# Kernel tuning notes

Hardware: AMD Instinct MI355X
Metric: run time of the kernel (lower is better)

Reference implementation:

```python
import jax, jax.numpy as jnp
import numpy as np

N = 50000      # nodes (B-rep faces)
E = 800000     # directed edges (avg degree 16)
F_IN = 9       # 8 surface-type flags + is_feature
H1, H2, C = 512, 128, 2


def setup_inputs() -> dict:
    key = jax.random.key(0)
    ks = jax.random.split(key, 8)
    x = jax.random.normal(ks[0], (N, F_IN), dtype=jnp.float32)
    edge_index = jax.random.randint(ks[1], (2, E), 0, N, dtype=jnp.int64)
    W1 = jax.random.normal(ks[2], (F_IN, H1), dtype=jnp.float32) / np.sqrt(F_IN)
    b1 = jnp.zeros((H1,), dtype=jnp.float32)
    W2 = jax.random.normal(ks[3], (H1, H2), dtype=jnp.float32) / np.sqrt(H1)
    b2 = jnp.zeros((H2,), dtype=jnp.float32)
    W3 = jax.random.normal(ks[4], (H2, C), dtype=jnp.float32) / np.sqrt(H2)
    b3 = jnp.zeros((C,), dtype=jnp.float32)
    return {"x": x, "W1": W1, "b1": b1, "W2": W2, "b2": b2,
            "W3": W3, "b3": b3, "edge_index": edge_index}


def reference(x, W1, b1, W2, b2, W3, b3, edge_index):
    n = x.shape[0]
    self_idx = jnp.arange(n, dtype=edge_index.dtype)
    # GCN with self-loops and symmetric normalization (PyG gcn_norm)
    src = jnp.concatenate([edge_index[0], self_idx])  # [E+N]
    dst = jnp.concatenate([edge_index[1], self_idx])  # [E+N]
    deg = jax.ops.segment_sum(jnp.ones_like(src, dtype=x.dtype), dst, num_segments=n)
    dinv = jnp.where(deg > 0, jax.lax.rsqrt(jnp.maximum(deg, 1.0)), 0.0)
    norm = dinv[src] * dinv[dst]  # [E+N]

    def gcn(h, W, b):
        h = h @ W                                   # [N, out]
        msg = h[src] * norm[:, None]                # gather + scale
        return jax.ops.segment_sum(msg, dst, num_segments=n) + b  # scatter-add

    h = jax.nn.relu(gcn(x, W1, b1))
    h = jax.nn.relu(gcn(h, W2, b2))
    # F.dropout with training=False is identity (inference mode)
    h = gcn(h, W3, b3)
    return jax.nn.log_softmax(h, axis=1)
```

## Files before the change

### kernel.cpp

```cpp
#include <hip/hip_runtime.h>
#include <hip/hip_bf16.h>

typedef __attribute__((ext_vector_type(8))) short short8;
typedef __attribute__((ext_vector_type(4))) float float4v;
typedef unsigned int uint;

#define NBLK 192

static __device__ __forceinline__ float2 up_bf2(uint v) {
    float2 r;
    r.x = __uint_as_float(v << 16);
    r.y = __uint_as_float(v & 0xffff0000u);
    return r;
}
static __device__ __forceinline__ short f2bf_bits(float x) {
    union { __hip_bfloat16 h; short s; } u;
    u.h = __float2bfloat16(x);
    return u.s;
}


__global__ __launch_bounds__(256) void k_hist(const int* __restrict__ dst, int E, int chunk,
        int shift, int nbuck, int* __restrict__ histBlk) {
    __shared__ int h[256];
    h[threadIdx.x] = 0;
    __syncthreads();
    int blk = blockIdx.x;
    int e0 = blk * chunk, e1 = min(E, e0 + chunk);
    for (int e = e0 + threadIdx.x; e < e1; e += 256)
        atomicAdd(&h[dst[e] >> shift], 1);
    __syncthreads();
    if (threadIdx.x < nbuck) histBlk[threadIdx.x * NBLK + blk] = h[threadIdx.x];
}


__global__ __launch_bounds__(256) void k_btot(const int* __restrict__ histBlk,
                                              int* __restrict__ btot) {
    __shared__ int s[256];
    int b = blockIdx.x, t = threadIdx.x;
    s[t] = (t < NBLK) ? histBlk[b * NBLK + t] : 0;
    __syncthreads();
    for (int off = 128; off; off >>= 1) {
        if (t < off) s[t] += s[t + off];
        __syncthreads();
    }
    if (t == 0) btot[b] = s[0];
}


__global__ __launch_bounds__(256) void k_bscan(const int* __restrict__ histBlk,
        const int* __restrict__ btot, int nbuck,
        int* __restrict__ baseBlk, int* __restrict__ bucketBase) {
    __shared__ int s[256], sb[256];
    int b = blockIdx.x, t = threadIdx.x;
    int v = (t < NBLK) ? histBlk[b * NBLK + t] : 0;
    s[t] = v;
    sb[t] = (t < nbuck) ? btot[t] : 0;
    __syncthreads();
    for (int off = 1; off < 256; off <<= 1) {
        int u = (t >= off) ? s[t - off] : 0;
        int u2 = (t >= off) ? sb[t - off] : 0;
        __syncthreads();
        s[t] += u;
        sb[t] += u2;
        __syncthreads();
    }
    int base = (b > 0) ? sb[b - 1] : 0;
    if (t < NBLK) baseBlk[b * NBLK + t] = base + s[t] - v;
    if (t == 0) bucketBase[b] = base;
}


__global__ __launch_bounds__(256) void k_scatterbin(const int* __restrict__ src,
        const int* __restrict__ dst, int E, int chunk, int shift, int nbuck,
        const int* __restrict__ baseBlk, uint* __restrict__ binned) {
    __shared__ int cur[256];
    int blk = blockIdx.x;
    if (threadIdx.x < nbuck) cur[threadIdx.x] = baseBlk[threadIdx.x * NBLK + blk];
    __syncthreads();
    int e0 = blk * chunk, e1 = min(E, e0 + chunk);
    int mask = (1 << shift) - 1;
    for (int e = e0 + threadIdx.x; e < e1; e += 256) {
        int d = dst[e];
        int pos = atomicAdd(&cur[d >> shift], 1);
        binned[pos] = (uint)src[e] | ((uint)(d & mask) << 24);
    }
}


__global__ __launch_bounds__(256) void k_csrbuild(const uint* __restrict__ binned,
        const int* __restrict__ bucketBase, const float* __restrict__ x,
        int E, int shift, int n, int nbuck,
        int* __restrict__ row_ptr, float* __restrict__ dinv, float* __restrict__ xs,
        int* __restrict__ csr) {
    __shared__ int cnt[256], lcur[256];
    int b = blockIdx.x, t = threadIdx.x;
    cnt[t] = 0;
    __syncthreads();
    int lo = bucketBase[b];
    int hi = (b + 1 < nbuck) ? bucketBase[b + 1] : E;
    for (int e = lo + t; e < hi; e += 256)
        atomicAdd(&cnt[binned[e] >> 24], 1);
    __syncthreads();
    int c = cnt[t];
    lcur[t] = c;
    __syncthreads();
    for (int off = 1; off < 256; off <<= 1) {
        int u = (t >= off) ? lcur[t - off] : 0;
        __syncthreads();
        lcur[t] += u;
        __syncthreads();
    }
    int node0 = b << shift;
    int nodeEnd = min(n, (b + 1) << shift);
    int cntNodes = nodeEnd - node0;
    int myBase = lo + lcur[t] - c;
    if (t < cntNodes) {
        row_ptr[node0 + t] = myBase;
        dinv[node0 + t] = rsqrtf((float)(c + 1));
    }
    if (b == nbuck - 1 && t == 0) row_ptr[n] = E;
    for (int j = t; j < cntNodes * 9; j += 256) {
        int nl = j / 9, f = j - nl * 9;
        float dnl = rsqrtf((float)(cnt[nl] + 1));
        xs[(size_t)(node0 + nl) * 9 + f] = dnl * x[(size_t)(node0 + nl) * 9 + f];
    }
    __syncthreads();
    lcur[t] = myBase;
    __syncthreads();
    for (int e = lo + t; e < hi; e += 256) {
        uint p = binned[e];
        int pos = atomicAdd(&lcur[p >> 24], 1);
        csr[pos] = (int)(p & 0xFFFFFF);
    }
}


__global__ __launch_bounds__(256) void k_agg1(const float* __restrict__ xs,
                       const float* __restrict__ dinv,
                       const int* __restrict__ row_ptr, const int* __restrict__ csr,
                       float* __restrict__ aggx, int n) {
    int node = blockIdx.x * 16 + (threadIdx.x >> 4);
    if (node >= n) return;
    int f = threadIdx.x & 15;
    bool act = f < 9;
    float acc = act ? xs[node * 9 + f] : 0.f;
    int e0 = row_ptr[node], e1 = row_ptr[node + 1];
    int e = e0;
    for (; e + 4 <= e1; e += 4) {
        int s0 = csr[e], s1 = csr[e + 1], s2 = csr[e + 2], s3 = csr[e + 3];
        float x0 = act ? xs[s0 * 9 + f] : 0.f;
        float x1 = act ? xs[s1 * 9 + f] : 0.f;
        float x2 = act ? xs[s2 * 9 + f] : 0.f;
        float x3 = act ? xs[s3 * 9 + f] : 0.f;
        acc += (x0 + x1) + (x2 + x3);
    }
    for (; e < e1; ++e) {
        int sA = csr[e];
        acc += act ? xs[sA * 9 + f] : 0.f;
    }
    if (act) aggx[node * 9 + f] = dinv[node] * acc;
}

__global__ __launch_bounds__(512, 2) void k_l12(const float* __restrict__ aggx,
                       const float* __restrict__ W1, const float* __restrict__ b1,
                       const float* __restrict__ W2, const float* __restrict__ dinv,
                       __hip_bfloat16* __restrict__ t2, int n, int ntile) {
    __shared__ short bsh[64 * 128 * 8];
    int t = threadIdx.x;

    for (int idx = t; idx < 64 * 128; idx += 512) {
        int kb = idx >> 7, c = idx & 127;
        const float* wp = W2 + (size_t)(kb * 8) * 128 + c;
        short8 o;
#pragma unroll
        for (int j = 0; j < 8; ++j) o[j] = f2bf_bits(wp[j * 128]);
        *reinterpret_cast<short8*>(bsh + (size_t)idx * 8) = o;
    }
    __syncthreads();

    int wid = t >> 6, lane = t & 63;
    int tile = blockIdx.x * 8 + wid;
    if (tile >= ntile) return;
    int r = lane & 15, quad = lane >> 4;
    int m0 = tile << 4;

    const float* ap = aggx + (size_t)(m0 + r) * 9;
    float4 a0 = *(const float4*)ap;
    float4 a1 = *(const float4*)(ap + 4);
    float av[9] = {a0.x, a0.y, a0.z, a0.w, a1.x, a1.y, a1.z, a1.w, ap[8]};

    float4v acc[8];
#pragma unroll
    for (int cg = 0; cg < 8; ++cg) acc[cg] = (float4v){0, 0, 0, 0};

#pragma unroll
    for (int kt = 0; kt < 16; ++kt) {
        int kb = kt * 32 + quad * 8;
        float4 bb0 = *(const float4*)(b1 + kb);
        float4 bb1 = *(const float4*)(b1 + kb + 4);
        float a8[8] = {bb0.x, bb0.y, bb0.z, bb0.w, bb1.x, bb1.y, bb1.z, bb1.w};
#pragma unroll
        for (int f = 0; f < 9; ++f) {
            const float* wp = W1 + f * 512 + kb;
            float4 wa = *(const float4*)wp;
            float4 wb = *(const float4*)(wp + 4);
            float xv = av[f];
            a8[0] += xv * wa.x; a8[1] += xv * wa.y; a8[2] += xv * wa.z; a8[3] += xv * wa.w;
            a8[4] += xv * wb.x; a8[5] += xv * wb.y; a8[6] += xv * wb.z; a8[7] += xv * wb.w;
        }
        short8 afr;
#pragma unroll
        for (int j = 0; j < 8; ++j) afr[j] = f2bf_bits(fmaxf(a8[j], 0.f));

#pragma unroll
        for (int cg = 0; cg < 8; ++cg) {
            short8 b = *reinterpret_cast<const short8*>(
                bsh + (size_t)(((kt * 4 + quad) * 128) + cg * 16 + r) * 8);
            acc[cg] = __builtin_amdgcn_mfma_f32_16x16x32_bf16(afr, b, acc[cg], 0, 0, 0);
        }
    }

#pragma unroll
    for (int i = 0; i < 4; ++i) {
        int node = m0 + quad * 4 + i;
        if (node < n) {
            float di = dinv[node];
            __hip_bfloat16* op = t2 + (size_t)node * 128 + r;
#pragma unroll
            for (int cg = 0; cg < 8; ++cg)
                op[cg * 16] = __float2bfloat16(di * acc[cg][i]);
        }
    }
}


__global__ __launch_bounds__(256) void k_agg2(const uint* __restrict__ t2u,
                       const float* __restrict__ dinv,
                       const int* __restrict__ row_ptr, const int* __restrict__ csr,
                       const float* __restrict__ b2, const float* __restrict__ W3,
                       float2* __restrict__ t3, int n) {
    int node = blockIdx.x * 4 + (threadIdx.x >> 6);
    if (node >= n) return;
    int lane = threadIdx.x & 63;
    float2 p = up_bf2(t2u[(size_t)node * 64 + lane]);
    float a0 = p.x, a1 = p.y;
    int e0 = row_ptr[node], e1 = row_ptr[node + 1];
    int e = e0;
    for (; e + 8 <= e1; e += 8) {
        int si[8];
        uint ri[8];
#pragma unroll
        for (int j = 0; j < 8; ++j) si[j] = csr[e + j];
#pragma unroll
        for (int j = 0; j < 8; ++j) ri[j] = t2u[(size_t)si[j] * 64 + lane];
#pragma unroll
        for (int j = 0; j < 8; ++j) {
            float2 q = up_bf2(ri[j]);
            a0 += q.x;
            a1 += q.y;
        }
    }
    for (; e + 2 <= e1; e += 2) {
        int s0 = csr[e], s1 = csr[e + 1];
        uint r0 = t2u[(size_t)s0 * 64 + lane];
        uint r1 = t2u[(size_t)s1 * 64 + lane];
        float2 q0 = up_bf2(r0), q1 = up_bf2(r1);
        a0 += q0.x + q1.x;
        a1 += q0.y + q1.y;
    }
    if (e < e1) {
        float2 q0 = up_bf2(t2u[(size_t)csr[e] * 64 + lane]);
        a0 += q0.x;
        a1 += q0.y;
    }
    float di = dinv[node];
    float2 bb = *reinterpret_cast<const float2*>(b2 + 2 * lane);
    float h0 = fmaxf(di * a0 + bb.x, 0.f);
    float h1v = fmaxf(di * a1 + bb.y, 0.f);
    float4 wv = *reinterpret_cast<const float4*>(W3 + 4 * lane);
    float c0 = h0 * wv.x + h1v * wv.z;
    float c1 = h0 * wv.y + h1v * wv.w;
#pragma unroll
    for (int off = 32; off; off >>= 1) {
        c0 += __shfl_xor(c0, off);
        c1 += __shfl_xor(c1, off);
    }
    if (lane == 0) t3[node] = make_float2(di * c0, di * c1);
}


__global__ void k_agg3(const float2* __restrict__ t3, const float* __restrict__ dinv,
                       const int* __restrict__ row_ptr, const int* __restrict__ csr,
                       const float* __restrict__ b3, float2* __restrict__ outv, int n) {
    int node = blockIdx.x * blockDim.x + threadIdx.x;
    if (node >= n) return;
    float2 s = t3[node];
    float a0 = s.x, a1 = s.y;
    int e0 = row_ptr[node], e1 = row_ptr[node + 1];
    int e = e0;
    for (; e + 4 <= e1; e += 4) {
        int s0 = csr[e], s1 = csr[e + 1], s2 = csr[e + 2], s3 = csr[e + 3];
        float2 q0 = t3[s0], q1 = t3[s1], q2 = t3[s2], q3 = t3[s3];
        a0 += q0.x + q1.x + q2.x + q3.x;
        a1 += q0.y + q1.y + q2.y + q3.y;
    }
    for (; e < e1; ++e) {
        float2 q0 = t3[csr[e]];
        a0 += q0.x;
        a1 += q0.y;
    }
    float di = dinv[node];
    float z0 = di * a0 + b3[0];
    float z1 = di * a1 + b3[1];
    float m = fmaxf(z0, z1);
    float lse = m + logf(expf(z0 - m) + expf(z1 - m));
    outv[node] = make_float2(z0 - lse, z1 - lse);
}


extern "C" void kernel_launch(void* const* d_in, const int* in_sizes, int n_in,
                              void* d_out, int out_size, void* d_ws, size_t ws_size,
                              hipStream_t stream) {
    const float* x  = (const float*)d_in[0];
    const float* W1 = (const float*)d_in[1];
    const float* b1 = (const float*)d_in[2];
    const float* W2 = (const float*)d_in[3];
    const float* b2 = (const float*)d_in[4];
    const float* W3 = (const float*)d_in[5];
    const float* b3 = (const float*)d_in[6];
    const int* edges = (const int*)d_in[7];

    int n = in_sizes[0] / 9;
    int E = in_sizes[7] / 2;
    const int* src = edges;
    const int* dst = edges + E;

    char* p = (char*)d_ws;
    auto alloc = [&](size_t bytes) {
        char* q = p;
        p += (bytes + 511) & ~(size_t)511;
        return q;
    };
    float* dinv       = (float*)alloc((size_t)n * 4);
    int*   row_ptr    = (int*)alloc((size_t)(n + 1) * 4);
    int*   csr        = (int*)alloc((size_t)E * 4);
    int*   histBlk    = (int*)alloc((size_t)256 * NBLK * 4);
    int*   baseBlk    = (int*)alloc((size_t)256 * NBLK * 4);
    int*   btot       = (int*)alloc(256 * 4);
    int*   bucketBase = (int*)alloc(256 * 4);
    uint*  binned     = (uint*)alloc((size_t)E * 4);
    float* xs         = (float*)alloc((size_t)n * 9 * 4);
    float* aggx       = (float*)alloc((size_t)(n + 64) * 9 * 4);
    __hip_bfloat16* t2 = (__hip_bfloat16*)alloc((size_t)n * 128 * 2);
    float2* t3 = (float2*)alloc((size_t)n * 8);

    const int B = 256;
    int shift = 8;
    int nbuck = ((n - 1) >> shift) + 1;
    int chunk = (E + NBLK - 1) / NBLK;

    k_hist<<<NBLK, B, 0, stream>>>(dst, E, chunk, shift, nbuck, histBlk);
    k_btot<<<nbuck, B, 0, stream>>>(histBlk, btot);
    k_bscan<<<nbuck, B, 0, stream>>>(histBlk, btot, nbuck, baseBlk, bucketBase);
    k_scatterbin<<<NBLK, B, 0, stream>>>(src, dst, E, chunk, shift, nbuck, baseBlk, binned);
    k_csrbuild<<<nbuck, B, 0, stream>>>(binned, bucketBase, x, E, shift, n, nbuck,
                                        row_ptr, dinv, xs, csr);

    k_agg1<<<(n + 15) / 16, B, 0, stream>>>(xs, dinv, row_ptr, csr, aggx, n);

    int ntile = (n + 15) / 16;
    k_l12<<<(ntile + 7) / 8, 512, 0, stream>>>(aggx, W1, b1, W2, dinv, t2, n, ntile);
    k_agg2<<<(n + 3) / 4, 256, 0, stream>>>((const uint*)t2, dinv, row_ptr, csr, b2, W3, t3, n);

    k_agg3<<<(n + B - 1) / B, B, 0, stream>>>(t3, dinv, row_ptr, csr, b3, (float2*)d_out, n);
}
```

Before: 218.2 us.

## Compute layer-1 linear on MFMA with bf16 aggregated input and pre-packed W1 fragments

The layer-1 9x512 transform inside k_l12 now runs on MFMA instructions instead of scalar FMAs. k_agg1 writes its output as zero-padded bf16 rows of 32 elements, and a new small kernel pre-packs W1 into MFMA B-fragment layout. The ReLU'd hidden tile is passed from accumulator layout to A-operand layout through a per-wave LDS buffer, and each wave now handles two 16-row tiles so the W2 LDS staging is amortised over more rows. This cuts the VALU work of the first layer. In exchange it adds LDS round trips, bf16 rounding of the layer-1 input, and one extra kernel launch.

```diff
diff --git a/kernel.cpp b/kernel.cpp
--- a/kernel.cpp
+++ b/kernel.cpp
@@ -139,7 +139,7 @@
 __global__ __launch_bounds__(256) void k_agg1(const float* __restrict__ xs,
                        const float* __restrict__ dinv,
                        const int* __restrict__ row_ptr, const int* __restrict__ csr,
-                       float* __restrict__ aggx, int n) {
+                       __hip_bfloat16* __restrict__ aggx_bf, int n) {
     int node = blockIdx.x * 16 + (threadIdx.x >> 4);
     if (node >= n) return;
     int f = threadIdx.x & 15;
@@ -159,14 +159,37 @@
         int sA = csr[e];
         acc += act ? xs[sA * 9 + f] : 0.f;
     }
-    if (act) aggx[node * 9 + f] = dinv[node] * acc;
-}
-
-__global__ __launch_bounds__(512, 2) void k_l12(const float* __restrict__ aggx,
-                       const float* __restrict__ W1, const float* __restrict__ b1,
+    float v = act ? dinv[node] * acc : 0.f;
+    __hip_bfloat16* op = aggx_bf + (size_t)node * 32;
+    union { __hip_bfloat16 h; short s; } u;
+    u.h = __float2bfloat16(v);
+    reinterpret_cast<short*>(op)[f] = u.s;
+    reinterpret_cast<short*>(op)[16 + f] = 0;
+}
+
+
+__global__ __launch_bounds__(256) void k_w1frag(const float* __restrict__ W1,
+                                                __hip_bfloat16* __restrict__ W1frag) {
+    int t = blockIdx.x * 256 + threadIdx.x;
+    if (t >= 32 * 64) return;
+    int ctile = t >> 6, lane = t & 63;
+    int col = ctile * 16 + (lane & 15);
+    int k0 = (lane >> 4) * 8;
+    short8 o;
+#pragma unroll
+    for (int j = 0; j < 8; ++j) {
+        int k = k0 + j;
+        o[j] = f2bf_bits(k < 9 ? W1[k * 512 + col] : 0.f);
+    }
+    *reinterpret_cast<short8*>(W1frag + (size_t)t * 8) = o;
+}
+
+__global__ __launch_bounds__(512, 2) void k_l12(const __hip_bfloat16* __restrict__ aggx_bf,
+                       const __hip_bfloat16* __restrict__ W1frag, const float* __restrict__ b1,
                        const float* __restrict__ W2, const float* __restrict__ dinv,
-                       __hip_bfloat16* __restrict__ t2, int n, int ntile) {
+                       __hip_bfloat16* __restrict__ t2, int n, int npair) {
     __shared__ short bsh[64 * 128 * 8];
+    __shared__ short h1s[8][16][40];
     int t = threadIdx.x;
 
     for (int idx = t; idx < 64 * 128; idx += 512) {
@@ -180,56 +203,57 @@
     __syncthreads();
 
     int wid = t >> 6, lane = t & 63;
-    int tile = blockIdx.x * 8 + wid;
-    if (tile >= ntile) return;
+    int pair = blockIdx.x * 8 + wid;
+    if (pair >= npair) return;
     int r = lane & 15, quad = lane >> 4;
-    int m0 = tile << 4;
-
-    const float* ap = aggx + (size_t)(m0 + r) * 9;
-    float4 a0 = *(const float4*)ap;
-    float4 a1 = *(const float4*)(ap + 4);
-    float av[9] = {a0.x, a0.y, a0.z, a0.w, a1.x, a1.y, a1.z, a1.w, ap[8]};
-
-    float4v acc[8];
-#pragma unroll
-    for (int cg = 0; cg < 8; ++cg) acc[cg] = (float4v){0, 0, 0, 0};
-
-#pragma unroll
-    for (int kt = 0; kt < 16; ++kt) {
-        int kb = kt * 32 + quad * 8;
-        float4 bb0 = *(const float4*)(b1 + kb);
-        float4 bb1 = *(const float4*)(b1 + kb + 4);
-        float a8[8] = {bb0.x, bb0.y, bb0.z, bb0.w, bb1.x, bb1.y, bb1.z, bb1.w};
-#pragma unroll
-        for (int f = 0; f < 9; ++f) {
-            const float* wp = W1 + f * 512 + kb;
-            float4 wa = *(const float4*)wp;
-            float4 wb = *(const float4*)(wp + 4);
-            float xv = av[f];
-            a8[0] += xv * wa.x; a8[1] += xv * wa.y; a8[2] += xv * wa.z; a8[3] += xv * wa.w;
-            a8[4] += xv * wb.x; a8[5] += xv * wb.y; a8[6] += xv * wb.z; a8[7] += xv * wb.w;
+    short (*hs)[40] = h1s[wid];
+
+#pragma unroll
+    for (int half = 0; half < 2; ++half) {
+        int m0 = (pair << 5) + half * 16;
+        short8 aagg = *reinterpret_cast<const short8*>(
+            aggx_bf + (size_t)(m0 + r) * 32 + quad * 8);
+
+        float4v acc[8];
+#pragma unroll
+        for (int cg = 0; cg < 8; ++cg) acc[cg] = (float4v){0, 0, 0, 0};
+
+        for (int kt = 0; kt < 16; ++kt) {
+            short8 bf0 = *reinterpret_cast<const short8*>(
+                W1frag + ((size_t)(2 * kt) * 64 + lane) * 8);
+            short8 bf1 = *reinterpret_cast<const short8*>(
+                W1frag + ((size_t)(2 * kt + 1) * 64 + lane) * 8);
+            float4v c0 = __builtin_amdgcn_mfma_f32_16x16x32_bf16(
+                aagg, bf0, (float4v){0, 0, 0, 0}, 0, 0, 0);
+            float4v c1 = __builtin_amdgcn_mfma_f32_16x16x32_bf16(
+                aagg, bf1, (float4v){0, 0, 0, 0}, 0, 0, 0);
+            float bb0 = b1[kt * 32 + r];
+            float bb1 = b1[kt * 32 + 16 + r];
+#pragma unroll
+            for (int i = 0; i < 4; ++i) {
+                int row = quad * 4 + i;
+                hs[row][r]      = f2bf_bits(fmaxf(c0[i] + bb0, 0.f));
+                hs[row][16 + r] = f2bf_bits(fmaxf(c1[i] + bb1, 0.f));
+            }
+            short8 am = *reinterpret_cast<const short8*>(&hs[r][quad * 8]);
+#pragma unroll
+            for (int cg = 0; cg < 8; ++cg) {
+                short8 b = *reinterpret_cast<const short8*>(
+                    bsh + (size_t)(((kt * 4 + quad) * 128) + cg * 16 + r) * 8);
+                acc[cg] = __builtin_amdgcn_mfma_f32_16x16x32_bf16(am, b, acc[cg], 0, 0, 0);
+            }
         }
-        short8 afr;
-#pragma unroll
-        for (int j = 0; j < 8; ++j) afr[j] = f2bf_bits(fmaxf(a8[j], 0.f));
-
-#pragma unroll
-        for (int cg = 0; cg < 8; ++cg) {
-            short8 b = *reinterpret_cast<const short8*>(
-                bsh + (size_t)(((kt * 4 + quad) * 128) + cg * 16 + r) * 8);
-            acc[cg] = __builtin_amdgcn_mfma_f32_16x16x32_bf16(afr, b, acc[cg], 0, 0, 0);
-        }
-    }
-
-#pragma unroll
-    for (int i = 0; i < 4; ++i) {
-        int node = m0 + quad * 4 + i;
-        if (node < n) {
-            float di = dinv[node];
-            __hip_bfloat16* op = t2 + (size_t)node * 128 + r;
-#pragma unroll
-            for (int cg = 0; cg < 8; ++cg)
-                op[cg * 16] = __float2bfloat16(di * acc[cg][i]);
+
+#pragma unroll
+        for (int i = 0; i < 4; ++i) {
+            int node = m0 + quad * 4 + i;
+            if (node < n) {
+                float di = dinv[node];
+                __hip_bfloat16* op = t2 + (size_t)node * 128 + r;
+#pragma unroll
+                for (int cg = 0; cg < 8; ++cg)
+                    op[cg * 16] = __float2bfloat16(di * acc[cg][i]);
+            }
         }
     }
 }
@@ -351,7 +375,8 @@
     int*   bucketBase = (int*)alloc(256 * 4);
     uint*  binned     = (uint*)alloc((size_t)E * 4);
     float* xs         = (float*)alloc((size_t)n * 9 * 4);
-    float* aggx       = (float*)alloc((size_t)(n + 64) * 9 * 4);
+    __hip_bfloat16* aggx_bf = (__hip_bfloat16*)alloc((size_t)(n + 64) * 32 * 2);
+    __hip_bfloat16* W1frag  = (__hip_bfloat16*)alloc((size_t)32 * 64 * 8 * 2);
     __hip_bfloat16* t2 = (__hip_bfloat16*)alloc((size_t)n * 128 * 2);
     float2* t3 = (float2*)alloc((size_t)n * 8);
 
@@ -367,10 +392,12 @@
     k_csrbuild<<<nbuck, B, 0, stream>>>(binned, bucketBase, x, E, shift, n, nbuck,
                                         row_ptr, dinv, xs, csr);
 
-    k_agg1<<<(n + 15) / 16, B, 0, stream>>>(xs, dinv, row_ptr, csr, aggx, n);
+    k_w1frag<<<8, B, 0, stream>>>(W1, W1frag);
+    k_agg1<<<(n + 15) / 16, B, 0, stream>>>(xs, dinv, row_ptr, csr, aggx_bf, n);
 
     int ntile = (n + 15) / 16;
-    k_l12<<<(ntile + 7) / 8, 512, 0, stream>>>(aggx, W1, b1, W2, dinv, t2, n, ntile);
+    int npair = (ntile + 1) / 2;
+    k_l12<<<(npair + 7) / 8, 512, 0, stream>>>(aggx_bf, W1frag, b1, W2, dinv, t2, n, npair);
     k_agg2<<<(n + 3) / 4, 256, 0, stream>>>((const uint*)t2, dinv, row_ptr, csr, b2, W3, t3, n);
 
     k_agg3<<<(n + B - 1) / B, B, 0, stream>>>(t3, dinv, row_ptr, csr, b3, (float2*)d_out, n);
```

Measured after the change: 194.6 us (median of 2 runs). 1.12x faster.
